# Optimization experiments

Hardware: AMD Instinct MI355X
Metric: run time of the kernel (lower is better)

The kernel has to match this reference:

```python
import jax, jax.numpy as jnp
import numpy as np

N, IN_DIM, OUT_DIM, H = 4096, 128, 128, 4
HEAD_DIM = OUT_DIM // H
NEG_SLOPE = 0.2


def setup_inputs() -> dict:
    key = jax.random.key(0)
    k1, k2, k3, k4, k5 = jax.random.split(key, 5)
    x = jax.random.normal(k1, (N, IN_DIM), dtype=jnp.float32)
    adj = jax.random.randint(k2, (N, N), 0, 2, dtype=jnp.int32)
    # nn.Linear(in_dim, out_dim, bias=False): weight is [out_dim, in_dim]
    W = jax.random.normal(k3, (OUT_DIM, IN_DIM), dtype=jnp.float32) * (1.0 / np.sqrt(IN_DIM))
    attn_src = jax.random.normal(k4, (1, H, HEAD_DIM), dtype=jnp.float32) * 0.1
    attn_dst = jax.random.normal(k5, (1, H, HEAD_DIM), dtype=jnp.float32) * 0.1
    return {"x": x, "adj": adj, "W": W, "attn_src": attn_src, "attn_dst": attn_dst}


def reference(x, adj, W, attn_src, attn_dst):
    n = x.shape[0]
    h = (x @ W.T).reshape(n, H, HEAD_DIM)            # [N, H, D]
    e_src = jnp.sum(h * attn_src, axis=-1)           # [N, H]
    e_dst = jnp.sum(h * attn_dst, axis=-1)           # [N, H]
    e = e_src[:, None, :] + e_dst[None, :, :]        # [N, N, H]
    e = jax.nn.leaky_relu(e, negative_slope=NEG_SLOPE)
    e = jnp.where((adj == 0)[:, :, None], -jnp.inf, e)
    alpha = jax.nn.softmax(e, axis=1)                # softmax over neighbors j
    # dropout omitted (eval mode)
    out = jnp.einsum('ijh,jhd->ihd', alpha, h)       # [N, H, D]
    return out.reshape(n, -1)
```

## Files before the change

### kernel.cpp

```cpp
#include <hip/hip_runtime.h>
#include <hip/hip_bf16.h>

#define NN 4096
#define SJ 8
#define JCH (NN / SJ)
#define JSTEP 64
#define NSTEPS (JCH / JSTEP)
#define LOG2E 1.44269504f

typedef __attribute__((ext_vector_type(4))) float f32x4;
typedef __attribute__((ext_vector_type(4))) int i32x4;
typedef __attribute__((ext_vector_type(4))) unsigned int u32x4;
typedef __attribute__((ext_vector_type(8))) short short8;

__device__ __forceinline__ unsigned pk2(float a, float b) {
    float2 t; t.x = a; t.y = b;
    __hip_bfloat162 h = __float22bfloat162_rn(t);
    unsigned r;
    __builtin_memcpy(&r, &h, 4);
    return r;
}

__device__ __forceinline__ short8 load8_bf(const float* __restrict__ p) {
    f32x4 a = *(const f32x4*)p;
    f32x4 b = *(const f32x4*)(p + 4);
    u32x4 v = {pk2(a[0], a[1]), pk2(a[2], a[3]), pk2(b[0], b[1]), pk2(b[2], b[3])};
    return __builtin_bit_cast(short8, v);
}

__global__ __launch_bounds__(256) void k1_proj(
        const float* __restrict__ x, const float* __restrict__ W,
        const float* __restrict__ asrc, const float* __restrict__ adst,
        unsigned short* __restrict__ hT, float* __restrict__ Rt,
        unsigned* __restrict__ BDt) {
    __shared__ unsigned short ttile[4][32][16];
    const int ibase = blockIdx.x * 16;
    const int w = threadIdx.x >> 6;
    const int lane = threadIdx.x & 63;
    const int grp = lane >> 4, li = lane & 15;

    const float* xrow = x + (ibase + li) * 128;
    const float* w0 = W + (w * 32 + li) * 128;
    const float* w1 = W + (w * 32 + 16 + li) * 128;

    f32x4 c0 = {0.f, 0.f, 0.f, 0.f}, c1 = {0.f, 0.f, 0.f, 0.f};
#pragma unroll
    for (int ko = 0; ko < 128; ko += 32) {
        const int kk = ko + grp * 8;
        short8 a = load8_bf(xrow + kk);
        short8 b0 = load8_bf(w0 + kk);
        short8 b1 = load8_bf(w1 + kk);
        c0 = __builtin_amdgcn_mfma_f32_16x16x32_bf16(a, b0, c0, 0, 0, 0);
        c1 = __builtin_amdgcn_mfma_f32_16x16x32_bf16(a, b1, c1, 0, 0, 0);
    }
    const float as0 = asrc[w * 32 + li], as1 = asrc[w * 32 + 16 + li];
    const float ad0 = adst[w * 32 + li], ad1 = adst[w * 32 + 16 + li];
    float pes[4], ped[4];
#pragma unroll
    for (int r = 0; r < 4; ++r) {
        pes[r] = c0[r] * as0 + c1[r] * as1;
        ped[r] = c0[r] * ad0 + c1[r] * ad1;
    }
#pragma unroll
    for (int m = 1; m < 16; m <<= 1) {
#pragma unroll
        for (int r = 0; r < 4; ++r) {
            pes[r] += __shfl_xor(pes[r], m);
            ped[r] += __shfl_xor(ped[r], m);
        }
    }
    if (li == 0) {
#pragma unroll
        for (int r = 0; r < 4; ++r) {
            const int row = ibase + grp * 4 + r;
            Rt[w * NN + row] = __builtin_amdgcn_exp2f(-0.8f * LOG2E * pes[r]);
            const float Bv = __builtin_amdgcn_exp2f(LOG2E * ped[r]);
            const float Dv = __builtin_amdgcn_exp2f(0.2f * LOG2E * ped[r]);
            BDt[w * NN + row] = pk2(Bv, Dv);
        }
    }
    unsigned short* tw = &ttile[w][0][0];
    {
        uint2 v0; v0.x = pk2(c0[0], c0[1]); v0.y = pk2(c0[2], c0[3]);
        uint2 v1; v1.x = pk2(c1[0], c1[1]); v1.y = pk2(c1[2], c1[3]);
        *(uint2*)&tw[li * 16 + grp * 4] = v0;
        *(uint2*)&tw[(li + 16) * 16 + grp * 4] = v1;
    }
    __syncthreads();
    const int d = lane >> 1, half = lane & 1;
    u32x4 v = *(const u32x4*)&ttile[w][d][half * 8];
    *(u32x4*)(hT + (size_t)(w * 32 + d) * NN + ibase + half * 8) = v;
}

struct SR {
    short8 t00, t01, t10, t11;
    u32x4 b0a, b0b, b1a, b1b;
};

__device__ __forceinline__ short8 buildQ(float R, const u32x4 ba, const u32x4 bb,
                                         const i32x4 alo, const i32x4 ahi) {
    float p[8];
#pragma unroll
    for (int e = 0; e < 4; ++e) {
        const unsigned v = ba[e];
        const float B = __builtin_bit_cast(float, v << 16);
        const float D = __builtin_bit_cast(float, v & 0xFFFF0000u);
        const float m = fmaxf(B, R * D);
        p[e] = __builtin_bit_cast(float, __builtin_bit_cast(unsigned, m) & (0u - (unsigned)alo[e]));
    }
#pragma unroll
    for (int e = 0; e < 4; ++e) {
        const unsigned v = bb[e];
        const float B = __builtin_bit_cast(float, v << 16);
        const float D = __builtin_bit_cast(float, v & 0xFFFF0000u);
        const float m = fmaxf(B, R * D);
        p[4 + e] = __builtin_bit_cast(float, __builtin_bit_cast(unsigned, m) & (0u - (unsigned)ahi[e]));
    }
    u32x4 u = {pk2(p[0], p[1]), pk2(p[2], p[3]), pk2(p[4], p[5]), pk2(p[6], p[7])};
    return __builtin_bit_cast(short8, u);
}

__global__ __launch_bounds__(256) void k3_main(
        const int* __restrict__ adj, const unsigned short* __restrict__ hT,
        const float* __restrict__ Rt, const unsigned* __restrict__ BDt,
        float* __restrict__ numer, float* __restrict__ denom) {
    __shared__ unsigned int adjbuf[3][32 * 64];

    const int ibase = blockIdx.x * 32;
    const int jstart = blockIdx.y * JCH;
    const int head = threadIdx.x >> 6;
    const int lane = threadIdx.x & 63;
    const int grp = lane >> 4, li = lane & 15;
    const int sub = lane >> 4, p = lane & 15;

    const float R0 = Rt[head * NN + ibase + li];
    const float R1 = Rt[head * NN + ibase + 16 + li];
    const unsigned short* h0 = hT + (size_t)(head * 32 + li) * NN;
    const unsigned short* h1 = hT + (size_t)(head * 32 + 16 + li) * NN;
    const unsigned* bd = BDt + head * NN;
    const unsigned int* adju = (const unsigned int*)adj;

    f32x4 c00 = {0.f,0.f,0.f,0.f}, c01 = {0.f,0.f,0.f,0.f};
    f32x4 c10 = {0.f,0.f,0.f,0.f}, c11 = {0.f,0.f,0.f,0.f};
    f32x4 dn0 = {0.f,0.f,0.f,0.f}, dn1 = {0.f,0.f,0.f,0.f};
    short8 bones;
#pragma unroll
    for (int e = 0; e < 8; ++e) bones[e] = (short)0x3F80;

    auto stage = [&](unsigned int* dst, int jb) {
#pragma unroll
        for (int k = 0; k < 2; ++k) {
            const int Rw = head * 8 + k * 4 + sub;
            const int c = p ^ (Rw & 15);
            const unsigned int* g = adju + (size_t)(ibase + Rw) * NN + jb + c * 4;
            __builtin_amdgcn_global_load_lds(g, dst + (head * 8 + k * 4) * 64, 16, 0, 0);
        }
    };
    auto loadR = [&](int jb) {
        SR r;
        r.t00 = *(const short8*)(h0 + jb + grp * 8);
        r.t01 = *(const short8*)(h0 + jb + 32 + grp * 8);
        r.t10 = *(const short8*)(h1 + jb + grp * 8);
        r.t11 = *(const short8*)(h1 + jb + 32 + grp * 8);
        r.b0a = *(const u32x4*)(bd + jb + grp * 8);
        r.b0b = *(const u32x4*)(bd + jb + grp * 8 + 4);
        r.b1a = *(const u32x4*)(bd + jb + 32 + grp * 8);
        r.b1b = *(const u32x4*)(bd + jb + 32 + grp * 8 + 4);
        return r;
    };

    unsigned int* bA = &adjbuf[0][0];
    unsigned int* bB = &adjbuf[1][0];
    unsigned int* bC = &adjbuf[2][0];

    stage(bA, jstart);
    SR Rg = loadR(jstart);
    stage(bB, jstart + JSTEP);
    asm volatile("s_waitcnt vmcnt(2)" ::: "memory");
    __builtin_amdgcn_s_barrier();

    for (int t = 0; t < NSTEPS; ++t) {
        const int jb = jstart + t * JSTEP;
        SR Rn = Rg;
        if (t + 1 < NSTEPS) Rn = loadR(jb + JSTEP);
        if (t + 2 < NSTEPS) stage(bC, jb + 2 * JSTEP);

#pragma unroll
        for (int ks = 0; ks < 2; ++ks) {
            const short8 tA = ks ? Rg.t01 : Rg.t00;
            const short8 tB = ks ? Rg.t11 : Rg.t10;
            const u32x4 ba = ks ? Rg.b1a : Rg.b0a;
            const u32x4 bb = ks ? Rg.b1b : Rg.b0b;
            const int cb = ks * 8 + grp * 2;
            const i32x4 q00 = *(const i32x4*)&bA[li * 64 + (cb ^ li) * 4];
            const i32x4 q01 = *(const i32x4*)&bA[li * 64 + ((cb + 1) ^ li) * 4];
            const i32x4 q10 = *(const i32x4*)&bA[(li + 16) * 64 + (cb ^ li) * 4];
            const i32x4 q11 = *(const i32x4*)&bA[(li + 16) * 64 + ((cb + 1) ^ li) * 4];

            const short8 A0 = buildQ(R0, ba, bb, q00, q01);
            const short8 A1 = buildQ(R1, ba, bb, q10, q11);

            c00 = __builtin_amdgcn_mfma_f32_16x16x32_bf16(A0, tA, c00, 0, 0, 0);
            c01 = __builtin_amdgcn_mfma_f32_16x16x32_bf16(A0, tB, c01, 0, 0, 0);
            c10 = __builtin_amdgcn_mfma_f32_16x16x32_bf16(A1, tA, c10, 0, 0, 0);
            c11 = __builtin_amdgcn_mfma_f32_16x16x32_bf16(A1, tB, c11, 0, 0, 0);
            dn0 = __builtin_amdgcn_mfma_f32_16x16x32_bf16(A0, bones, dn0, 0, 0, 0);
            dn1 = __builtin_amdgcn_mfma_f32_16x16x32_bf16(A1, bones, dn1, 0, 0, 0);
        }

        asm volatile("s_waitcnt vmcnt(2)" ::: "memory");
        __builtin_amdgcn_s_barrier();
        unsigned int* tmp = bA; bA = bB; bB = bC; bC = tmp;
        Rg = Rn;
    }

    const int r0 = ibase + grp * 4;
    float* nb = numer + head * 32 + li;
#pragma unroll
    for (int r = 0; r < 4; ++r) {
        atomicAdd(nb + (size_t)(r0 + r) * 128, c00[r]);
        atomicAdd(nb + (size_t)(r0 + r) * 128 + 16, c01[r]);
        atomicAdd(nb + (size_t)(r0 + 16 + r) * 128, c10[r]);
        atomicAdd(nb + (size_t)(r0 + 16 + r) * 128 + 16, c11[r]);
    }
    if (li == 0) {
#pragma unroll
        for (int r = 0; r < 4; ++r) {
            atomicAdd(denom + (r0 + r) * 4 + head, dn0[r]);
            atomicAdd(denom + (r0 + 16 + r) * 4 + head, dn1[r]);
        }
    }
}

__global__ __launch_bounds__(256) void k4_fin(const float* __restrict__ numer,
                                              const float* __restrict__ denom,
                                              float* __restrict__ out) {
    const int idx = blockIdx.x * 256 + threadIdx.x;
    const int node = idx >> 7;
    const int headc = (idx & 127) >> 5;
    out[idx] = numer[idx] / denom[node * 4 + headc];
}

extern "C" void kernel_launch(void* const* d_in, const int* in_sizes, int n_in,
                              void* d_out, int out_size, void* d_ws, size_t ws_size,
                              hipStream_t stream) {
    const float* x = (const float*)d_in[0];
    const int* adj = (const int*)d_in[1];
    const float* W = (const float*)d_in[2];
    const float* asrc = (const float*)d_in[3];
    const float* adst = (const float*)d_in[4];
    float* out = (float*)d_out;

    char* ws = (char*)d_ws;
    float* numer = (float*)ws;
    float* denom = (float*)(ws + (size_t)2097152);
    float* Rt = (float*)(ws + (size_t)2097152 + 65536);
    unsigned* BDt = (unsigned*)(ws + (size_t)2097152 + 131072);
    unsigned short* hT = (unsigned short*)(ws + (size_t)2097152 + 196608);

    (void)hipMemsetAsync(numer, 0, 2097152 + 65536, stream);
    k1_proj<<<256, 256, 0, stream>>>(x, W, asrc, adst, hT, Rt, BDt);
    k3_main<<<dim3(128, SJ), 256, 0, stream>>>(adj, hT, Rt, BDt, numer, denom);
    k4_fin<<<2048, 256, 0, stream>>>(numer, denom, out);
}
```

Measured before the change: 57.93 us.

## Halve row tile to 16 rows per block and fully unroll pipelined j-loop

Cuts each block's i-tile from 32 to 16 rows, so the grid doubles and each wave issues one A fragment and three MFMAs per k-step instead of six. The adjacency staging shrinks to one async global-to-LDS load per thread, and the j-loop is fully unrolled with explicit buffer indices, a launch-bounds occupancy hint and sched barriers. The aim is higher occupancy and lower register pressure. The cost is that each loaded hT/BD tile is reused across half as many rows, doubling that traffic, and the number of atomic adds doubles.

```diff
diff --git a/kernel.cpp b/kernel.cpp
--- a/kernel.cpp
+++ b/kernel.cpp
@@ -6,6 +6,7 @@
 #define JCH (NN / SJ)
 #define JSTEP 64
 #define NSTEPS (JCH / JSTEP)
+#define ROWS 16
 #define LOG2E 1.44269504f
 
 typedef __attribute__((ext_vector_type(4))) float f32x4;
@@ -98,7 +99,7 @@
 };
 
 __device__ __forceinline__ short8 buildQ(float R, const u32x4 ba, const u32x4 bb,
-                                         const i32x4 alo, const i32x4 ahi) {
+                                         const i32x4 q0, const i32x4 q1) {
     float p[8];
 #pragma unroll
     for (int e = 0; e < 4; ++e) {
@@ -106,7 +107,7 @@
         const float B = __builtin_bit_cast(float, v << 16);
         const float D = __builtin_bit_cast(float, v & 0xFFFF0000u);
         const float m = fmaxf(B, R * D);
-        p[e] = __builtin_bit_cast(float, __builtin_bit_cast(unsigned, m) & (0u - (unsigned)alo[e]));
+        p[e] = __builtin_bit_cast(float, __builtin_bit_cast(unsigned, m) & (0u - (unsigned)q0[e]));
     }
 #pragma unroll
     for (int e = 0; e < 4; ++e) {
@@ -114,121 +115,107 @@
         const float B = __builtin_bit_cast(float, v << 16);
         const float D = __builtin_bit_cast(float, v & 0xFFFF0000u);
         const float m = fmaxf(B, R * D);
-        p[4 + e] = __builtin_bit_cast(float, __builtin_bit_cast(unsigned, m) & (0u - (unsigned)ahi[e]));
+        p[4 + e] = __builtin_bit_cast(float, __builtin_bit_cast(unsigned, m) & (0u - (unsigned)q1[e]));
     }
     u32x4 u = {pk2(p[0], p[1]), pk2(p[2], p[3]), pk2(p[4], p[5]), pk2(p[6], p[7])};
     return __builtin_bit_cast(short8, u);
 }
 
-__global__ __launch_bounds__(256) void k3_main(
+__global__ __launch_bounds__(256, 4) void k3_main(
         const int* __restrict__ adj, const unsigned short* __restrict__ hT,
         const float* __restrict__ Rt, const unsigned* __restrict__ BDt,
         float* __restrict__ numer, float* __restrict__ denom) {
-    __shared__ unsigned int adjbuf[3][32 * 64];
-
-    const int ibase = blockIdx.x * 32;
+    __shared__ unsigned int adjbuf[3][ROWS * 64];
+
+    const int ibase = blockIdx.x * ROWS;
     const int jstart = blockIdx.y * JCH;
     const int head = threadIdx.x >> 6;
     const int lane = threadIdx.x & 63;
     const int grp = lane >> 4, li = lane & 15;
-    const int sub = lane >> 4, p = lane & 15;
-
-    const float R0 = Rt[head * NN + ibase + li];
-    const float R1 = Rt[head * NN + ibase + 16 + li];
-    const unsigned short* h0 = hT + (size_t)(head * 32 + li) * NN;
-    const unsigned short* h1 = hT + (size_t)(head * 32 + 16 + li) * NN;
-    const unsigned* bd = BDt + head * NN;
+
+    const float Rv = Rt[head * NN + ibase + li];
+    const unsigned short* h0 = hT + (size_t)(head * 32 + li) * NN + jstart;
+    const unsigned short* h1 = hT + (size_t)(head * 32 + 16 + li) * NN + jstart;
+    const unsigned* bd = BDt + head * NN + jstart;
     const unsigned int* adju = (const unsigned int*)adj;
 
-    f32x4 c00 = {0.f,0.f,0.f,0.f}, c01 = {0.f,0.f,0.f,0.f};
-    f32x4 c10 = {0.f,0.f,0.f,0.f}, c11 = {0.f,0.f,0.f,0.f};
-    f32x4 dn0 = {0.f,0.f,0.f,0.f}, dn1 = {0.f,0.f,0.f,0.f};
+    const int srow = head * 4 + grp;
+    const unsigned int* gsrc = adju + (size_t)(ibase + srow) * NN + jstart + (li ^ srow) * 4;
+
+    f32x4 c0 = {0.f,0.f,0.f,0.f}, c1 = {0.f,0.f,0.f,0.f}, dn = {0.f,0.f,0.f,0.f};
     short8 bones;
 #pragma unroll
     for (int e = 0; e < 8; ++e) bones[e] = (short)0x3F80;
 
-    auto stage = [&](unsigned int* dst, int jb) {
-#pragma unroll
-        for (int k = 0; k < 2; ++k) {
-            const int Rw = head * 8 + k * 4 + sub;
-            const int c = p ^ (Rw & 15);
-            const unsigned int* g = adju + (size_t)(ibase + Rw) * NN + jb + c * 4;
-            __builtin_amdgcn_global_load_lds(g, dst + (head * 8 + k * 4) * 64, 16, 0, 0);
-        }
+    auto stage = [&](int slot, int toff) {
+        __builtin_amdgcn_global_load_lds(gsrc + toff, &adjbuf[slot][head * 4 * 64], 16, 0, 0);
     };
-    auto loadR = [&](int jb) {
+    auto loadR = [&](int toff) {
         SR r;
-        r.t00 = *(const short8*)(h0 + jb + grp * 8);
-        r.t01 = *(const short8*)(h0 + jb + 32 + grp * 8);
-        r.t10 = *(const short8*)(h1 + jb + grp * 8);
-        r.t11 = *(const short8*)(h1 + jb + 32 + grp * 8);
-        r.b0a = *(const u32x4*)(bd + jb + grp * 8);
-        r.b0b = *(const u32x4*)(bd + jb + grp * 8 + 4);
-        r.b1a = *(const u32x4*)(bd + jb + 32 + grp * 8);
-        r.b1b = *(const u32x4*)(bd + jb + 32 + grp * 8 + 4);
+        r.t00 = *(const short8*)(h0 + toff + grp * 8);
+        r.t01 = *(const short8*)(h0 + toff + 32 + grp * 8);
+        r.t10 = *(const short8*)(h1 + toff + grp * 8);
+        r.t11 = *(const short8*)(h1 + toff + 32 + grp * 8);
+        r.b0a = *(const u32x4*)(bd + toff + grp * 8);
+        r.b0b = *(const u32x4*)(bd + toff + grp * 8 + 4);
+        r.b1a = *(const u32x4*)(bd + toff + 32 + grp * 8);
+        r.b1b = *(const u32x4*)(bd + toff + 32 + grp * 8 + 4);
         return r;
     };
-
-    unsigned int* bA = &adjbuf[0][0];
-    unsigned int* bB = &adjbuf[1][0];
-    unsigned int* bC = &adjbuf[2][0];
-
-    stage(bA, jstart);
-    SR Rg = loadR(jstart);
-    stage(bB, jstart + JSTEP);
-    asm volatile("s_waitcnt vmcnt(2)" ::: "memory");
+    auto compute = [&](const unsigned int* buf, const SR& S) {
+#pragma unroll
+        for (int ks = 0; ks < 2; ++ks) {
+            const short8 tA = ks ? S.t01 : S.t00;
+            const short8 tB = ks ? S.t11 : S.t10;
+            const u32x4 ba = ks ? S.b1a : S.b0a;
+            const u32x4 bb = ks ? S.b1b : S.b0b;
+            const int cb = ks * 8 + grp * 2;
+            const i32x4 q0 = *(const i32x4*)&buf[li * 64 + (cb ^ li) * 4];
+            const i32x4 q1 = *(const i32x4*)&buf[li * 64 + ((cb + 1) ^ li) * 4];
+            const short8 A = buildQ(Rv, ba, bb, q0, q1);
+            c0 = __builtin_amdgcn_mfma_f32_16x16x32_bf16(A, tA, c0, 0, 0, 0);
+            c1 = __builtin_amdgcn_mfma_f32_16x16x32_bf16(A, tB, c1, 0, 0, 0);
+            dn = __builtin_amdgcn_mfma_f32_16x16x32_bf16(A, bones, dn, 0, 0, 0);
+        }
+    };
+
+    SR S[2];
+    stage(0, 0);
+    S[0] = loadR(0);
+    stage(1, JSTEP);
+    asm volatile("s_waitcnt vmcnt(1)" ::: "memory");
     __builtin_amdgcn_s_barrier();
-
+    __builtin_amdgcn_sched_barrier(0);
+
+#pragma unroll
     for (int t = 0; t < NSTEPS; ++t) {
-        const int jb = jstart + t * JSTEP;
-        SR Rn = Rg;
-        if (t + 1 < NSTEPS) Rn = loadR(jb + JSTEP);
-        if (t + 2 < NSTEPS) stage(bC, jb + 2 * JSTEP);
-
-#pragma unroll
-        for (int ks = 0; ks < 2; ++ks) {
-            const short8 tA = ks ? Rg.t01 : Rg.t00;
-            const short8 tB = ks ? Rg.t11 : Rg.t10;
-            const u32x4 ba = ks ? Rg.b1a : Rg.b0a;
-            const u32x4 bb = ks ? Rg.b1b : Rg.b0b;
-            const int cb = ks * 8 + grp * 2;
-            const i32x4 q00 = *(const i32x4*)&bA[li * 64 + (cb ^ li) * 4];
-            const i32x4 q01 = *(const i32x4*)&bA[li * 64 + ((cb + 1) ^ li) * 4];
-            const i32x4 q10 = *(const i32x4*)&bA[(li + 16) * 64 + (cb ^ li) * 4];
-            const i32x4 q11 = *(const i32x4*)&bA[(li + 16) * 64 + ((cb + 1) ^ li) * 4];
-
-            const short8 A0 = buildQ(R0, ba, bb, q00, q01);
-            const short8 A1 = buildQ(R1, ba, bb, q10, q11);
-
-            c00 = __builtin_amdgcn_mfma_f32_16x16x32_bf16(A0, tA, c00, 0, 0, 0);
-            c01 = __builtin_amdgcn_mfma_f32_16x16x32_bf16(A0, tB, c01, 0, 0, 0);
-            c10 = __builtin_amdgcn_mfma_f32_16x16x32_bf16(A1, tA, c10, 0, 0, 0);
-            c11 = __builtin_amdgcn_mfma_f32_16x16x32_bf16(A1, tB, c11, 0, 0, 0);
-            dn0 = __builtin_amdgcn_mfma_f32_16x16x32_bf16(A0, bones, dn0, 0, 0, 0);
-            dn1 = __builtin_amdgcn_mfma_f32_16x16x32_bf16(A1, bones, dn1, 0, 0, 0);
-        }
-
-        asm volatile("s_waitcnt vmcnt(2)" ::: "memory");
-        __builtin_amdgcn_s_barrier();
-        unsigned int* tmp = bA; bA = bB; bB = bC; bC = tmp;
-        Rg = Rn;
+        if (t + 1 < NSTEPS) S[(t + 1) & 1] = loadR((t + 1) * JSTEP);
+        if (t + 2 < NSTEPS) stage((t + 2) % 3, (t + 2) * JSTEP);
+
+        compute(&adjbuf[t % 3][0], S[t & 1]);
+
+        if (t + 2 < NSTEPS) {
+            asm volatile("s_waitcnt vmcnt(1)" ::: "memory");
+        } else if (t + 1 < NSTEPS) {
+            asm volatile("s_waitcnt vmcnt(0)" ::: "memory");
+        }
+        if (t + 1 < NSTEPS) {
+            __builtin_amdgcn_s_barrier();
+            __builtin_amdgcn_sched_barrier(0);
+        }
     }
 
     const int r0 = ibase + grp * 4;
     float* nb = numer + head * 32 + li;
 #pragma unroll
     for (int r = 0; r < 4; ++r) {
-        atomicAdd(nb + (size_t)(r0 + r) * 128, c00[r]);
-        atomicAdd(nb + (size_t)(r0 + r) * 128 + 16, c01[r]);
-        atomicAdd(nb + (size_t)(r0 + 16 + r) * 128, c10[r]);
-        atomicAdd(nb + (size_t)(r0 + 16 + r) * 128 + 16, c11[r]);
+        atomicAdd(nb + (size_t)(r0 + r) * 128, c0[r]);
+        atomicAdd(nb + (size_t)(r0 + r) * 128 + 16, c1[r]);
     }
     if (li == 0) {
 #pragma unroll
-        for (int r = 0; r < 4; ++r) {
-            atomicAdd(denom + (r0 + r) * 4 + head, dn0[r]);
-            atomicAdd(denom + (r0 + 16 + r) * 4 + head, dn1[r]);
-        }
+        for (int r = 0; r < 4; ++r)
+            atomicAdd(denom + (r0 + r) * 4 + head, dn[r]);
     }
 }
 
@@ -260,6 +247,6 @@
 
     (void)hipMemsetAsync(numer, 0, 2097152 + 65536, stream);
     k1_proj<<<256, 256, 0, stream>>>(x, W, asrc, adst, hT, Rt, BDt);
-    k3_main<<<dim3(128, SJ), 256, 0, stream>>>(adj, hT, Rt, BDt, numer, denom);
+    k3_main<<<dim3(NN / ROWS, SJ), 256, 0, stream>>>(adj, hT, Rt, BDt, numer, denom);
     k4_fin<<<2048, 256, 0, stream>>>(numer, denom, out);
 }
```

New measurement: 66.73 us. +15.2%, slower.

## Hand-schedule main loop with inline-asm loads and explicit double-buffered registers

Applied to the files above, without the earlier changes.

Replaces the compiler-generated loads of transposed features and B/D factors with inline-asm global_load_dwordx4 using immediate offsets. Precomputed base pointers cut per-iteration address arithmetic. The main loop is fully unrolled with ping-pong register sets, sched_barriers and explicit vmcnt waits, so the next tile's loads stay in flight during the MFMA work. This pins instruction order and the memory-wait counts, at the cost of more registers and fragile manual wait accounting.

```diff
diff --git a/kernel.cpp b/kernel.cpp
--- a/kernel.cpp
+++ b/kernel.cpp
@@ -92,13 +92,37 @@
     *(u32x4*)(hT + (size_t)(w * 32 + d) * NN + ibase + half * 8) = v;
 }
 
-struct SR {
-    short8 t00, t01, t10, t11;
-    u32x4 b0a, b0b, b1a, b1b;
-};
+__device__ __forceinline__ u32x4 gld0(const void* p) {
+    u32x4 d; asm volatile("global_load_dwordx4 %0, %1, off" : "=&v"(d) : "v"(p)); return d;
+}
+__device__ __forceinline__ u32x4 gld16(const void* p) {
+    u32x4 d; asm volatile("global_load_dwordx4 %0, %1, off offset:16" : "=&v"(d) : "v"(p)); return d;
+}
+__device__ __forceinline__ u32x4 gld64(const void* p) {
+    u32x4 d; asm volatile("global_load_dwordx4 %0, %1, off offset:64" : "=&v"(d) : "v"(p)); return d;
+}
+__device__ __forceinline__ u32x4 gld128(const void* p) {
+    u32x4 d; asm volatile("global_load_dwordx4 %0, %1, off offset:128" : "=&v"(d) : "v"(p)); return d;
+}
+__device__ __forceinline__ u32x4 gld144(const void* p) {
+    u32x4 d; asm volatile("global_load_dwordx4 %0, %1, off offset:144" : "=&v"(d) : "v"(p)); return d;
+}
+
+struct SR { u32x4 h0k0, h0k1, h1k0, h1k1, bd00, bd01, bd10, bd11; };
+
+#define LOADR(dst, toff) do {                                             \
+    (dst).h0k0 = gld0(h0b + (toff));  (dst).h0k1 = gld64(h0b + (toff));   \
+    (dst).h1k0 = gld0(h1b + (toff));  (dst).h1k1 = gld64(h1b + (toff));   \
+    (dst).bd00 = gld0(bd + (toff));   (dst).bd01 = gld16(bd + (toff));    \
+    (dst).bd10 = gld128(bd + (toff)); (dst).bd11 = gld144(bd + (toff));   \
+} while (0)
+
+#define LAUNDER(s) asm volatile("" : "+v"((s).h0k0), "+v"((s).h0k1),      \
+    "+v"((s).h1k0), "+v"((s).h1k1), "+v"((s).bd00), "+v"((s).bd01),       \
+    "+v"((s).bd10), "+v"((s).bd11))
 
 __device__ __forceinline__ short8 buildQ(float R, const u32x4 ba, const u32x4 bb,
-                                         const i32x4 alo, const i32x4 ahi) {
+                                         const i32x4 q0, const i32x4 q1) {
     float p[8];
 #pragma unroll
     for (int e = 0; e < 4; ++e) {
@@ -106,7 +130,7 @@
         const float B = __builtin_bit_cast(float, v << 16);
         const float D = __builtin_bit_cast(float, v & 0xFFFF0000u);
         const float m = fmaxf(B, R * D);
-        p[e] = __builtin_bit_cast(float, __builtin_bit_cast(unsigned, m) & (0u - (unsigned)alo[e]));
+        p[e] = __builtin_bit_cast(float, __builtin_bit_cast(unsigned, m) & (0u - (unsigned)q0[e]));
     }
 #pragma unroll
     for (int e = 0; e < 4; ++e) {
@@ -114,7 +138,7 @@
         const float B = __builtin_bit_cast(float, v << 16);
         const float D = __builtin_bit_cast(float, v & 0xFFFF0000u);
         const float m = fmaxf(B, R * D);
-        p[4 + e] = __builtin_bit_cast(float, __builtin_bit_cast(unsigned, m) & (0u - (unsigned)ahi[e]));
+        p[4 + e] = __builtin_bit_cast(float, __builtin_bit_cast(unsigned, m) & (0u - (unsigned)q1[e]));
     }
     u32x4 u = {pk2(p[0], p[1]), pk2(p[2], p[3]), pk2(p[4], p[5]), pk2(p[6], p[7])};
     return __builtin_bit_cast(short8, u);
@@ -131,14 +155,17 @@
     const int head = threadIdx.x >> 6;
     const int lane = threadIdx.x & 63;
     const int grp = lane >> 4, li = lane & 15;
-    const int sub = lane >> 4, p = lane & 15;
 
     const float R0 = Rt[head * NN + ibase + li];
     const float R1 = Rt[head * NN + ibase + 16 + li];
-    const unsigned short* h0 = hT + (size_t)(head * 32 + li) * NN;
-    const unsigned short* h1 = hT + (size_t)(head * 32 + 16 + li) * NN;
-    const unsigned* bd = BDt + head * NN;
+    const unsigned short* h0b = hT + (size_t)(head * 32 + li) * NN + jstart + grp * 8;
+    const unsigned short* h1b = h0b + (size_t)16 * NN;
+    const unsigned* bd = BDt + head * NN + jstart + grp * 8;
     const unsigned int* adju = (const unsigned int*)adj;
+
+    const int Rw0 = head * 8 + grp, Rw1 = Rw0 + 4;
+    const unsigned int* g0 = adju + (size_t)(ibase + Rw0) * NN + jstart + (li ^ (Rw0 & 15)) * 4;
+    const unsigned int* g1 = adju + (size_t)(ibase + Rw1) * NN + jstart + (li ^ (Rw1 & 15)) * 4;
 
     f32x4 c00 = {0.f,0.f,0.f,0.f}, c01 = {0.f,0.f,0.f,0.f};
     f32x4 c10 = {0.f,0.f,0.f,0.f}, c11 = {0.f,0.f,0.f,0.f};
@@ -147,59 +174,24 @@
 #pragma unroll
     for (int e = 0; e < 8; ++e) bones[e] = (short)0x3F80;
 
-    auto stage = [&](unsigned int* dst, int jb) {
-#pragma unroll
-        for (int k = 0; k < 2; ++k) {
-            const int Rw = head * 8 + k * 4 + sub;
-            const int c = p ^ (Rw & 15);
-            const unsigned int* g = adju + (size_t)(ibase + Rw) * NN + jb + c * 4;
-            __builtin_amdgcn_global_load_lds(g, dst + (head * 8 + k * 4) * 64, 16, 0, 0);
-        }
+    auto stage = [&](int slot, int s) {
+        __builtin_amdgcn_global_load_lds(g0 + s * JSTEP, &adjbuf[slot][(head * 8) * 64], 16, 0, 0);
+        __builtin_amdgcn_global_load_lds(g1 + s * JSTEP, &adjbuf[slot][(head * 8 + 4) * 64], 16, 0, 0);
     };
-    auto loadR = [&](int jb) {
-        SR r;
-        r.t00 = *(const short8*)(h0 + jb + grp * 8);
-        r.t01 = *(const short8*)(h0 + jb + 32 + grp * 8);
-        r.t10 = *(const short8*)(h1 + jb + grp * 8);
-        r.t11 = *(const short8*)(h1 + jb + 32 + grp * 8);
-        r.b0a = *(const u32x4*)(bd + jb + grp * 8);
-        r.b0b = *(const u32x4*)(bd + jb + grp * 8 + 4);
-        r.b1a = *(const u32x4*)(bd + jb + 32 + grp * 8);
-        r.b1b = *(const u32x4*)(bd + jb + 32 + grp * 8 + 4);
-        return r;
-    };
-
-    unsigned int* bA = &adjbuf[0][0];
-    unsigned int* bB = &adjbuf[1][0];
-    unsigned int* bC = &adjbuf[2][0];
-
-    stage(bA, jstart);
-    SR Rg = loadR(jstart);
-    stage(bB, jstart + JSTEP);
-    asm volatile("s_waitcnt vmcnt(2)" ::: "memory");
-    __builtin_amdgcn_s_barrier();
-
-    for (int t = 0; t < NSTEPS; ++t) {
-        const int jb = jstart + t * JSTEP;
-        SR Rn = Rg;
-        if (t + 1 < NSTEPS) Rn = loadR(jb + JSTEP);
-        if (t + 2 < NSTEPS) stage(bC, jb + 2 * JSTEP);
-
+    auto compute = [&](const unsigned int* buf, const SR& S) {
 #pragma unroll
         for (int ks = 0; ks < 2; ++ks) {
-            const short8 tA = ks ? Rg.t01 : Rg.t00;
-            const short8 tB = ks ? Rg.t11 : Rg.t10;
-            const u32x4 ba = ks ? Rg.b1a : Rg.b0a;
-            const u32x4 bb = ks ? Rg.b1b : Rg.b0b;
+            const u32x4 ba = ks ? S.bd10 : S.bd00;
+            const u32x4 bb = ks ? S.bd11 : S.bd01;
+            const short8 tA = __builtin_bit_cast(short8, ks ? S.h0k1 : S.h0k0);
+            const short8 tB = __builtin_bit_cast(short8, ks ? S.h1k1 : S.h1k0);
             const int cb = ks * 8 + grp * 2;
-            const i32x4 q00 = *(const i32x4*)&bA[li * 64 + (cb ^ li) * 4];
-            const i32x4 q01 = *(const i32x4*)&bA[li * 64 + ((cb + 1) ^ li) * 4];
-            const i32x4 q10 = *(const i32x4*)&bA[(li + 16) * 64 + (cb ^ li) * 4];
-            const i32x4 q11 = *(const i32x4*)&bA[(li + 16) * 64 + ((cb + 1) ^ li) * 4];
-
+            const i32x4 q00 = *(const i32x4*)&buf[li * 64 + ((cb) ^ li) * 4];
+            const i32x4 q01 = *(const i32x4*)&buf[li * 64 + ((cb + 1) ^ li) * 4];
+            const i32x4 q10 = *(const i32x4*)&buf[(li + 16) * 64 + ((cb) ^ li) * 4];
+            const i32x4 q11 = *(const i32x4*)&buf[(li + 16) * 64 + ((cb + 1) ^ li) * 4];
             const short8 A0 = buildQ(R0, ba, bb, q00, q01);
             const short8 A1 = buildQ(R1, ba, bb, q10, q11);
-
             c00 = __builtin_amdgcn_mfma_f32_16x16x32_bf16(A0, tA, c00, 0, 0, 0);
             c01 = __builtin_amdgcn_mfma_f32_16x16x32_bf16(A0, tB, c01, 0, 0, 0);
             c10 = __builtin_amdgcn_mfma_f32_16x16x32_bf16(A1, tA, c10, 0, 0, 0);
@@ -207,11 +199,41 @@
             dn0 = __builtin_amdgcn_mfma_f32_16x16x32_bf16(A0, bones, dn0, 0, 0, 0);
             dn1 = __builtin_amdgcn_mfma_f32_16x16x32_bf16(A1, bones, dn1, 0, 0, 0);
         }
-
-        asm volatile("s_waitcnt vmcnt(2)" ::: "memory");
-        __builtin_amdgcn_s_barrier();
-        unsigned int* tmp = bA; bA = bB; bB = bC; bC = tmp;
-        Rg = Rn;
+    };
+
+    SR S0, S1;
+    stage(0, 0);
+    __builtin_amdgcn_sched_barrier(0);
+    LOADR(S0, 0);
+    __builtin_amdgcn_sched_barrier(0);
+    stage(1, 1);
+    __builtin_amdgcn_sched_barrier(0);
+    asm volatile("s_waitcnt vmcnt(2)" ::: "memory");
+    LAUNDER(S0);
+    __builtin_amdgcn_s_barrier();
+    __builtin_amdgcn_sched_barrier(0);
+
+#pragma unroll
+    for (int t = 0; t < NSTEPS; ++t) {
+        SR& Scur = (t & 1) ? S1 : S0;
+        SR& Snxt = (t & 1) ? S0 : S1;
+        if (t + 1 < NSTEPS) { LOADR(Snxt, (t + 1) * JSTEP); }
+        __builtin_amdgcn_sched_barrier(0);
+        if (t + 2 < NSTEPS) stage((t + 2) % 3, t + 2);
+        __builtin_amdgcn_sched_barrier(0);
+
+        compute(&adjbuf[t % 3][0], Scur);
+
+        if (t + 1 < NSTEPS) {
+            if (t + 2 < NSTEPS) {
+                asm volatile("s_waitcnt vmcnt(2)" ::: "memory");
+            } else {
+                asm volatile("s_waitcnt vmcnt(0)" ::: "memory");
+            }
+            LAUNDER(Snxt);
+            __builtin_amdgcn_s_barrier();
+            __builtin_amdgcn_sched_barrier(0);
+        }
     }
 
     const int r0 = ibase + grp * 4;
```

Result: no change. 57.45 us (-0.8%).
